# Optimization experiments

Hardware: AMD Instinct MI355X
Metric: run time of the kernel (lower is better)

## Reference

```python
import jax, jax.numpy as jnp
import numpy as np
import math

DIM = 768
HEADS = 12
HEAD_DIM = DIM // HEADS
SCALE_PARAM_INIT = 1.0 / math.sqrt(DIM)  # Scale(scale=1/sqrt(dim), init=1.0)


def cosine_norm(x, eps=1e-6):
    norm = jnp.maximum(jnp.linalg.norm(x, axis=-1, keepdims=True), eps)
    return x / norm


def setup_inputs() -> dict:
    key = jax.random.key(0)
    ks = jax.random.split(key, 6)
    B, N = 8, 1024
    x = jax.random.normal(ks[0], (B, N, DIM), dtype=jnp.float32)
    # torch nn.Linear weights are [out, in]; y = x @ W^T
    std = 1.0 / math.sqrt(DIM)
    Wq = jax.random.uniform(ks[1], (DIM, DIM), jnp.float32, -std, std)
    Wk = jax.random.uniform(ks[2], (DIM, DIM), jnp.float32, -std, std)
    Wv = jax.random.uniform(ks[3], (DIM, DIM), jnp.float32, -std, std)
    Wo = jax.random.uniform(ks[4], (DIM, DIM), jnp.float32, -std, std)
    # Scale param s: ones * scale, perturbed slightly for generality
    s_qk = SCALE_PARAM_INIT * (1.0 + 0.1 * jax.random.normal(ks[5], (HEADS, HEAD_DIM), jnp.float32))
    return {"x": x, "Wq": Wq, "Wk": Wk, "Wv": Wv, "Wo": Wo, "s_qk": s_qk}


def reference(x, Wq, Wk, Wv, Wo, s_qk):
    B, N, _ = x.shape
    # projections (torch Linear: x @ W^T)
    q = (x @ Wq.T).reshape(B, N, HEADS, HEAD_DIM)
    k = (x @ Wk.T).reshape(B, N, HEADS, HEAD_DIM)
    v = (x @ Wv.T).reshape(B, N, HEADS, HEAD_DIM)
    # effective scale = s * (init / scale)
    s_eff = s_qk * (1.0 / SCALE_PARAM_INIT)  # [H, D]
    q = cosine_norm(q) * s_eff  # broadcast over [B, N, H, D]
    k = cosine_norm(k) * s_eff
    scale = HEAD_DIM ** 0.5  # note: multiplies logits (nGPT-style)
    # [B, H, N, N]
    logits = jnp.einsum('bqhd,bkhd->bhqk', q, k) * scale
    attn = jax.nn.softmax(logits, axis=-1)
    out = jnp.einsum('bhqk,bkhd->bqhd', attn, v).reshape(B, N, HEADS * HEAD_DIM)
    return out @ Wo.T
```

## Files before the change

### kernel.cpp

```cpp
#include <hip/hip_runtime.h>
#include <hip/hip_bf16.h>
#include <math.h>

#define NDIM 768
#define NHEADS 12
#define HD 64
#define SEQ 1024
#define BATCH 8
#define MROWS (BATCH * SEQ)
#define SQRT_DIM 27.712812921102035f
#define LOG2E 1.4426950408889634f

typedef unsigned short u16;
typedef unsigned int u32;
typedef __attribute__((ext_vector_type(8))) short short8;
typedef __attribute__((ext_vector_type(4))) short bf16x4;
typedef __attribute__((ext_vector_type(4))) float f32x4;
typedef __attribute__((ext_vector_type(16))) float f32x16;

#define MFMA16(a, b, c) __builtin_amdgcn_mfma_f32_16x16x32_bf16(a, b, c, 0, 0, 0)
#define MFMA32(a, b, c) __builtin_amdgcn_mfma_f32_32x32x16_bf16(a, b, c, 0, 0, 0)

#if __has_builtin(__builtin_amdgcn_exp2f)
#define EXP2(x) __builtin_amdgcn_exp2f(x)
#else
#define EXP2(x) exp2f(x)
#endif

__device__ inline u16 f2bf(float f) {
    __hip_bfloat16 h = __float2bfloat16(f);
    return *reinterpret_cast<u16*>(&h);
}

__device__ inline u32 rne_pack(float a, float b) {
    u32 ua = __builtin_bit_cast(u32, a), ub = __builtin_bit_cast(u32, b);
    ua = (ua + 0x7fffu + ((ua >> 16) & 1u)) >> 16;
    ub = (ub + 0x7fffu + ((ub >> 16) & 1u)) >> 16;
    return (ub << 16) | ua;
}

__device__ inline void gl2lds16(const void* g, void* l) {
    __builtin_amdgcn_global_load_lds((const __attribute__((address_space(1))) void*)g,
                                     (__attribute__((address_space(3))) void*)l, 16, 0, 0);
}

__device__ inline void bar() {
    asm volatile("" ::: "memory");
    __builtin_amdgcn_s_barrier();
    asm volatile("" ::: "memory");
}
#define LGKM0 asm volatile("s_waitcnt lgkmcnt(0)" ::: "memory")
#define VM0   asm volatile("s_waitcnt vmcnt(0)" ::: "memory")

__global__ __launch_bounds__(256) void castall(const float* __restrict__ x,
                                               const float* __restrict__ Wq,
                                               const float* __restrict__ Wk,
                                               const float* __restrict__ Wv,
                                               const float* __restrict__ Wo,
                                               u16* __restrict__ xb,
                                               u16* __restrict__ Wqkv,
                                               u16* __restrict__ Wob) {
    const int WB = (NDIM * NDIM) / 1024;
    int blk = blockIdx.x;
    const float* s;
    u16* d;
    int base;
    if (blk < 6144) {
        s = x; d = xb; base = blk * 1024;
    } else {
        int wsel = (blk - 6144) / WB, r = (blk - 6144) % WB;
        base = r * 1024;
        if (wsel == 0)      { s = Wq; d = Wqkv; }
        else if (wsel == 1) { s = Wk; d = Wqkv + NDIM * NDIM; }
        else if (wsel == 2) { s = Wv; d = Wqkv + 2 * NDIM * NDIM; }
        else                { s = Wo; d = Wob; }
    }
    int i = base + threadIdx.x * 4;
    float4 v = *(const float4*)(s + i);
    uint2 o = make_uint2(rne_pack(v.x, v.y), rne_pack(v.z, v.w));
    *(uint2*)(d + i) = o;
}

__global__ __launch_bounds__(512, 2) void gemm256_qkv(const u16* __restrict__ A,
                                                      const u16* __restrict__ B,
                                                      u16* __restrict__ Vt,
                                                      const float* __restrict__ s_qk,
                                                      u16* __restrict__ Qdst,
                                                      u16* __restrict__ Kdst) {
    constexpr int K = NDIM;
    constexpr int NT = K / 64;
    __shared__ __align__(16) u16 As[2][2][128 * 64];
    __shared__ __align__(16) u16 Bs[2][2][128 * 64];

    const int t = threadIdx.x;
    const int wave = t >> 6, lane = t & 63;
    const int quad = lane >> 4, l16 = lane & 15;
    const int fx = l16 & 7;
    const int blk = blockIdx.x;

    const int srow = lane >> 3;
    const int schk = (lane & 7) ^ srow;
    auto stg = [&](const u16* src, u16* dst) {
#pragma unroll
        for (int it = 0; it < 2; ++it) {
            const int cb = it * 512 + wave * 64;
            const int r = (cb >> 3) + srow;
            gl2lds16(src + (size_t)r * K + schk * 8, (char*)dst + cb * 16);
        }
    };

    if (blk < 256) {
        const int wm = wave >> 2, wn = wave & 3;
        const int xcd = blk & 7, local = blk >> 3;
        const int bm = xcd * 1024 + (local >> 3) * 256;
        const int bn = (local & 7) * 256;

        f32x4 acc[8][4];
#pragma unroll
        for (int i = 0; i < 8; ++i)
#pragma unroll
            for (int j = 0; j < 4; ++j) acc[i][j] = (f32x4){0.f, 0.f, 0.f, 0.f};

        const u16* Ag = A + (size_t)bm * K;
        const u16* Bg = B + (size_t)bn * K;

        stg(Ag,                        As[0][0]);
        stg(Ag + (size_t)128 * K,      As[0][1]);
        stg(Bg,                        Bs[0][0]);
        stg(Bg + (size_t)128 * K,      Bs[0][1]);
        stg(Bg + 64,                   Bs[1][0]);
        stg(Bg + (size_t)128 * K + 64, Bs[1][1]);
        asm volatile("s_waitcnt vmcnt(4)" ::: "memory");
        bar();

        short8 a[4][2], b0[2][2], b1[2][2];
        const int rb0 = (wn & 1) * 64;

#pragma unroll 2
        for (int T = 0; T < NT; ++T) {
            const int db = T & 1;
            u16* Asl = As[db][wm];
            u16* Bsl = Bs[db][wn >> 1];
            const u16* An = Ag + (size_t)(T + 1) * 64;
            const u16* Bn = Bg + (size_t)(T + 2) * 64;

#pragma unroll
            for (int mi = 0; mi < 4; ++mi) {
                const int r = mi * 16 + l16;
#pragma unroll
                for (int kk = 0; kk < 2; ++kk)
                    a[mi][kk] = *(const short8*)&Asl[(r * 8 + ((kk * 4 + quad) ^ fx)) * 8];
            }
#pragma unroll
            for (int ni = 0; ni < 2; ++ni) {
                const int r = rb0 + ni * 16 + l16;
#pragma unroll
                for (int kk = 0; kk < 2; ++kk)
                    b0[ni][kk] = *(const short8*)&Bsl[(r * 8 + ((kk * 4 + quad) ^ fx)) * 8];
            }
            if (T + 1 < NT) stg(An, As[db ^ 1][0]);
            bar();
            LGKM0;
            __builtin_amdgcn_s_setprio(1);
#pragma unroll
            for (int kk = 0; kk < 2; ++kk)
#pragma unroll
                for (int mi = 0; mi < 4; ++mi)
#pragma unroll
                    for (int ni = 0; ni < 2; ++ni)
                        acc[mi][ni] = MFMA16(a[mi][kk], b0[ni][kk], acc[mi][ni]);
            __builtin_amdgcn_s_setprio(0);
            bar();

#pragma unroll
            for (int ni = 0; ni < 2; ++ni) {
                const int r = rb0 + (ni + 2) * 16 + l16;
#pragma unroll
                for (int kk = 0; kk < 2; ++kk)
                    b1[ni][kk] = *(const short8*)&Bsl[(r * 8 + ((kk * 4 + quad) ^ fx)) * 8];
            }
            if (T + 1 < NT) stg(An + (size_t)128 * K, As[db ^ 1][1]);
            bar();
            LGKM0;
            __builtin_amdgcn_s_setprio(1);
#pragma unroll
            for (int kk = 0; kk < 2; ++kk)
#pragma unroll
                for (int mi = 0; mi < 4; ++mi)
#pragma unroll
                    for (int ni = 0; ni < 2; ++ni)
                        acc[mi][ni + 2] = MFMA16(a[mi][kk], b1[ni][kk], acc[mi][ni + 2]);
            __builtin_amdgcn_s_setprio(0);
            bar();

#pragma unroll
            for (int mi = 0; mi < 4; ++mi) {
                const int r = (mi + 4) * 16 + l16;
#pragma unroll
                for (int kk = 0; kk < 2; ++kk)
                    a[mi][kk] = *(const short8*)&Asl[(r * 8 + ((kk * 4 + quad) ^ fx)) * 8];
            }
            if (T + 2 < NT) stg(Bn, Bs[db][0]);
            bar();
            LGKM0;
            __builtin_amdgcn_s_setprio(1);
#pragma unroll
            for (int kk = 0; kk < 2; ++kk)
#pragma unroll
                for (int mi = 0; mi < 4; ++mi)
#pragma unroll
                    for (int ni = 0; ni < 2; ++ni)
                        acc[mi + 4][ni + 2] = MFMA16(a[mi][kk], b1[ni][kk], acc[mi + 4][ni + 2]);
            __builtin_amdgcn_s_setprio(0);
            bar();

            if (T + 2 < NT) stg(Bn + (size_t)128 * K, Bs[db][1]);
            bar();
            __builtin_amdgcn_s_setprio(1);
#pragma unroll
            for (int kk = 0; kk < 2; ++kk)
#pragma unroll
                for (int mi = 0; mi < 4; ++mi)
#pragma unroll
                    for (int ni = 0; ni < 2; ++ni)
                        acc[mi + 4][ni] = MFMA16(a[mi][kk], b0[ni][kk], acc[mi + 4][ni]);
            __builtin_amdgcn_s_setprio(0);
            if (T + 2 < NT) {
                asm volatile("s_waitcnt vmcnt(4)" ::: "memory");
            } else {
                VM0;
            }
            bar();
        }

        const int cg = (bn + wn * 64) >> 6;
        if (cg >= 2 * NHEADS) {
            const int h = cg - 2 * NHEADS;
#pragma unroll
            for (int mi = 0; mi < 8; ++mi) {
                const int row = bm + wm * 128 + mi * 16 + quad * 4;
                const int bb = row >> 10, n0 = row & 1023;
#pragma unroll
                for (int ni = 0; ni < 4; ++ni) {
                    const int dd = ni * 16 + l16;
                    uint2 pk = make_uint2(rne_pack(acc[mi][ni][0], acc[mi][ni][1]),
                                          rne_pack(acc[mi][ni][2], acc[mi][ni][3]));
                    *(uint2*)(Vt + (((size_t)(bb * NHEADS + h) * HD + dd) << 10) + n0) = pk;
                }
            }
        } else {
            const bool isq = cg < NHEADS;
            const int h = isq ? cg : cg - NHEADS;
            u16* dst = isq ? Qdst : Kdst;
            const float ex = isq ? 8.f * LOG2E : 1.f;
            float sq[4];
#pragma unroll
            for (int ni = 0; ni < 4; ++ni)
                sq[ni] = s_qk[h * HD + ni * 16 + l16] * SQRT_DIM * ex;
#pragma unroll
            for (int mi = 0; mi < 8; ++mi)
#pragma unroll
                for (int r = 0; r < 4; ++r) {
                    float ss = 0.f;
#pragma unroll
                    for (int ni = 0; ni < 4; ++ni) ss += acc[mi][ni][r] * acc[mi][ni][r];
                    ss += __shfl_xor(ss, 1, 64);
                    ss += __shfl_xor(ss, 2, 64);
                    ss += __shfl_xor(ss, 4, 64);
                    ss += __shfl_xor(ss, 8, 64);
                    float inv = 1.f / fmaxf(sqrtf(ss), 1e-6f);
                    const int row = bm + wm * 128 + mi * 16 + quad * 4 + r;
                    const int bb = row >> 10, tok = row & 1023;
                    u16* o = dst + ((size_t)(bb * NHEADS + h) * SEQ + tok) * HD;
#pragma unroll
                    for (int ni = 0; ni < 4; ++ni)
                        o[ni * 16 + l16] = f2bf(acc[mi][ni][r] * sq[ni] * inv);
                }
        }
    } else {
        const int q = blk - 256;
        const int bm = (q >> 1) * 128;
        const int bn = 2048 + (q & 1) * 128;
        const int wm4 = wave >> 1, wn2 = wave & 1;
        const u16* Aq = A + (size_t)bm * K;
        const u16* Bq = B + (size_t)bn * K;

        f32x4 qa[2][4];
#pragma unroll
        for (int i = 0; i < 2; ++i)
#pragma unroll
            for (int j = 0; j < 4; ++j) qa[i][j] = (f32x4){0.f, 0.f, 0.f, 0.f};

        stg(Aq, As[0][0]);
        stg(Bq, Bs[0][0]);
        VM0;
        bar();
#pragma unroll 2
        for (int T = 0; T < NT; ++T) {
            const int db = T & 1;
            if (T + 1 < NT) {
                stg(Aq + (size_t)(T + 1) * 64, As[db ^ 1][0]);
                stg(Bq + (size_t)(T + 1) * 64, Bs[db ^ 1][0]);
            }
            const u16* Asl = As[db][0];
            const u16* Bsl = Bs[db][0];
            short8 af[2][2], bf[4][2];
#pragma unroll
            for (int mi = 0; mi < 2; ++mi) {
                const int r = wm4 * 32 + mi * 16 + l16;
#pragma unroll
                for (int kk = 0; kk < 2; ++kk)
                    af[mi][kk] = *(const short8*)&Asl[(r * 8 + ((kk * 4 + quad) ^ fx)) * 8];
            }
#pragma unroll
            for (int ni = 0; ni < 4; ++ni) {
                const int r = wn2 * 64 + ni * 16 + l16;
#pragma unroll
                for (int kk = 0; kk < 2; ++kk)
                    bf[ni][kk] = *(const short8*)&Bsl[(r * 8 + ((kk * 4 + quad) ^ fx)) * 8];
            }
            __builtin_amdgcn_s_setprio(1);
#pragma unroll
            for (int kk = 0; kk < 2; ++kk)
#pragma unroll
                for (int mi = 0; mi < 2; ++mi)
#pragma unroll
                    for (int ni = 0; ni < 4; ++ni)
                        qa[mi][ni] = MFMA16(af[mi][kk], bf[ni][kk], qa[mi][ni]);
            __builtin_amdgcn_s_setprio(0);
            VM0;
            bar();
        }
        const int h = 8 + (q & 1) * 2 + wn2;
#pragma unroll
        for (int mi = 0; mi < 2; ++mi) {
            const int row = bm + wm4 * 32 + mi * 16 + quad * 4;
            const int bb = row >> 10, n0 = row & 1023;
#pragma unroll
            for (int ni = 0; ni < 4; ++ni) {
                const int dd = ni * 16 + l16;
                uint2 pk = make_uint2(rne_pack(qa[mi][ni][0], qa[mi][ni][1]),
                                      rne_pack(qa[mi][ni][2], qa[mi][ni][3]));
                *(uint2*)(Vt + (((size_t)(bb * NHEADS + h) * HD + dd) << 10) + n0) = pk;
            }
        }
    }
}

template <int EPI>
__global__ __launch_bounds__(256) void gemm_bf16(const u16* __restrict__ A,
                                                 const u16* __restrict__ B,
                                                 void* __restrict__ C, int N,
                                                 const float* __restrict__ s_qk,
                                                 u16* __restrict__ Qdst,
                                                 u16* __restrict__ Kdst,
                                                 int NX) {
    constexpr int K = NDIM;
    constexpr int NKT = K / 32;
    __shared__ __align__(16) u16 As[2][4096];
    __shared__ __align__(16) u16 Bs[2][4096];
    const int t = threadIdx.x;
    const int wave = t >> 6, lane = t & 63;
    const int quad = lane >> 4, l16 = lane & 15;
    const int wx = (wave & 1) * 64, wy = (wave >> 1) * 64;
    const int blk = blockIdx.x;
    const int xcd = blk & 7, local = blk >> 3;
    const int bm = (xcd * 8 + local / NX) * 128;
    const int bn = (local % NX) * 128;

    f32x4 acc[4][4];
#pragma unroll
    for (int i = 0; i < 4; ++i)
#pragma unroll
        for (int j = 0; j < 4; ++j) acc[i][j] = (f32x4){0.f, 0.f, 0.f, 0.f};

    const int srl = lane >> 2;
    const int skc = (lane & 3) ^ ((lane >> 3) & 3);
    auto stage = [&](int k0, int bsel) {
#pragma unroll
        for (int it = 0; it < 2; ++it) {
            const int cb = it * 256 + wave * 64;
            const int row = (cb >> 6) * 16 + srl;
            gl2lds16(A + (size_t)(bm + row) * K + k0 + skc * 8,
                     (char*)As[bsel] + cb * 16);
            gl2lds16(B + (size_t)(bn + row) * K + k0 + skc * 8,
                     (char*)Bs[bsel] + cb * 16);
        }
    };
    const int fxor = (l16 >> 1) & 3;

    stage(0, 0);
#pragma unroll
    for (int kt = 0; kt < NKT; ++kt) {
        __syncthreads();
        if (kt + 1 < NKT) stage((kt + 1) * 32, (kt + 1) & 1);
        const int b = kt & 1;
        short8 af[4], bfr[4];
#pragma unroll
        for (int i = 0; i < 4; ++i)
            af[i] = *(const short8*)&As[b][
                ((((wy >> 4) + i) * 64 + l16 * 4 + (quad ^ fxor)) * 8)];
#pragma unroll
        for (int j = 0; j < 4; ++j)
            bfr[j] = *(const short8*)&Bs[b][
                ((((wx >> 4) + j) * 64 + l16 * 4 + (quad ^ fxor)) * 8)];
#pragma unroll
        for (int i = 0; i < 4; ++i)
#pragma unroll
            for (int j = 0; j < 4; ++j) acc[i][j] = MFMA16(af[i], bfr[j], acc[i][j]);
    }

    if constexpr (EPI == 0) {
#pragma unroll
        for (int i = 0; i < 4; ++i)
#pragma unroll
            for (int j = 0; j < 4; ++j)
#pragma unroll
                for (int r = 0; r < 4; ++r) {
                    const int row = bm + wy + i * 16 + quad * 4 + r;
                    const int col = bn + wx + j * 16 + l16;
                    ((float*)C)[(size_t)row * N + col] = acc[i][j][r];
                }
    }
}

__global__ __launch_bounds__(256) void attn_mfma(const u16* __restrict__ Qh,
                                                 const u16* __restrict__ Kh,
                                                 const u16* __restrict__ Vt,
                                                 u16* __restrict__ AO) {
    __shared__ __align__(16) u16 Ks[512 * 8];
    __shared__ __align__(16) u16 Vs[512 * 8];
    __shared__ __align__(16) u16 Ps[4 * 32 * 64];

    const int t = threadIdx.x;
    const int wave = t >> 6, lane = t & 63;
    const int l31 = lane & 31, half = lane >> 5;
    const int b = blockIdx.z, h = blockIdx.y, q0 = blockIdx.x * 128;
    const int bh = b * NHEADS + h;
    const u16* Kb = Kh + (size_t)bh * SEQ * HD;
    const u16* Vb = Vt + (size_t)bh * HD * SEQ;
    const int qb = q0 + wave * 32;
    const int pbase = wave * 2048 + l31 * 64;
    const int sw = (l31 & 15);

    short8 qf[4];
#pragma unroll
    for (int tt = 0; tt < 4; ++tt)
        qf[tt] = *(const short8*)(Qh + ((size_t)bh * SEQ + qb + l31) * HD +
                                  tt * 16 + half * 8);

    f32x16 o[2];
#pragma unroll
    for (int dt = 0; dt < 2; ++dt)
#pragma unroll
        for (int r = 0; r < 16; ++r) o[dt][r] = 0.f;
    float lp = 0.f;

    const int arl = lane >> 3;
    const int acc8 = (lane & 7) ^ arl;
    const int fx8 = l31 & 7;

    for (int j0 = 0; j0 < SEQ; j0 += 64) {
        __syncthreads();
#pragma unroll
        for (int it = 0; it < 2; ++it) {
            const int cb = it * 256 + wave * 64;
            const int r0 = (cb >> 6) * 8 + arl;
            gl2lds16(Kb + (size_t)(j0 + r0) * HD + acc8 * 8, (char*)Ks + cb * 16);
            gl2lds16(Vb + (size_t)r0 * SEQ + j0 + acc8 * 8, (char*)Vs + cb * 16);
        }
        asm volatile("s_waitcnt vmcnt(0)" ::: "memory");
        __syncthreads();

#pragma unroll
        for (int kt = 0; kt < 2; ++kt) {
            f32x16 sa;
#pragma unroll
            for (int r = 0; r < 16; ++r) sa[r] = 0.f;
#pragma unroll
            for (int tt = 0; tt < 4; ++tt) {
                short8 kf = *(const short8*)&Ks[
                    (((kt * 4 + (l31 >> 3)) * 64) + fx8 * 8 +
                     ((2 * tt + half) ^ fx8)) * 8];
                sa = MFMA32(kf, qf[tt], sa);
            }
#pragma unroll
            for (int rg = 0; rg < 4; ++rg) {
                float p0 = EXP2(sa[rg * 4 + 0]);
                float p1 = EXP2(sa[rg * 4 + 1]);
                float p2 = EXP2(sa[rg * 4 + 2]);
                float p3 = EXP2(sa[rg * 4 + 3]);
                lp += (p0 + p1) + (p2 + p3);
                uint2 pk = make_uint2(rne_pack(p0, p1), rne_pack(p2, p3));
                const int u = kt * 8 + rg * 2 + half;
                *(uint2*)&Ps[pbase + (u ^ sw) * 4] = pk;
            }
        }

#pragma unroll
        for (int k2 = 0; k2 < 4; ++k2) {
            const int u0 = k2 * 4 + half * 2;
            bf16x4 lo = *(const bf16x4*)&Ps[pbase + ((u0 + 0) ^ sw) * 4];
            bf16x4 hi = *(const bf16x4*)&Ps[pbase + ((u0 + 1) ^ sw) * 4];
            short8 pf = __builtin_shufflevector(lo, hi, 0, 1, 2, 3, 4, 5, 6, 7);
#pragma unroll
            for (int dt = 0; dt < 2; ++dt) {
                short8 vf = *(const short8*)&Vs[
                    (((dt * 4 + (l31 >> 3)) * 64) + fx8 * 8 +
                     ((2 * k2 + half) ^ fx8)) * 8];
                o[dt] = MFMA32(vf, pf, o[dt]);
            }
        }
    }

    const float invl = 1.f / (lp + __shfl_xor(lp, 32, 64));
    u16* ob = AO + (size_t)(b * SEQ + qb + l31) * NDIM + h * HD;
#pragma unroll
    for (int dt = 0; dt < 2; ++dt)
#pragma unroll
        for (int rg = 0; rg < 4; ++rg) {
            bf16x4 ok = {(short)f2bf(o[dt][rg * 4 + 0] * invl),
                         (short)f2bf(o[dt][rg * 4 + 1] * invl),
                         (short)f2bf(o[dt][rg * 4 + 2] * invl),
                         (short)f2bf(o[dt][rg * 4 + 3] * invl)};
            *(bf16x4*)(ob + dt * 32 + rg * 8 + half * 4) = ok;
        }
}

extern "C" void kernel_launch(void* const* d_in, const int* in_sizes, int n_in,
                              void* d_out, int out_size, void* d_ws, size_t ws_size,
                              hipStream_t stream) {
    const float* x    = (const float*)d_in[0];
    const float* Wq   = (const float*)d_in[1];
    const float* Wk   = (const float*)d_in[2];
    const float* Wv   = (const float*)d_in[3];
    const float* Wo   = (const float*)d_in[4];
    const float* s_qk = (const float*)d_in[5];
    float* out = (float*)d_out;

    char* w = (char*)d_ws;
    const size_t TE = (size_t)MROWS * NDIM;
    u16* xb   = (u16*)w;                    w += TE * 2;
    u16* Wqkv = (u16*)w;                    w += (size_t)3 * NDIM * NDIM * 2;
    u16* Wob  = (u16*)w;                    w += (size_t)NDIM * NDIM * 2;
    u16* Qh   = (u16*)w;                    w += TE * 2;
    u16* Kh   = (u16*)w;                    w += TE * 2;
    u16* Vt   = (u16*)w;                    w += TE * 2;
    u16* ao   = (u16*)w;

    castall<<<6144 + 4 * 576, 256, 0, stream>>>(x, Wq, Wk, Wv, Wo, xb, Wqkv, Wob);

    gemm256_qkv<<<384, 512, 0, stream>>>(xb, Wqkv, Vt, s_qk, Qh, Kh);

    attn_mfma<<<dim3(SEQ / 128, NHEADS, BATCH), 256, 0, stream>>>(Qh, Kh, Vt, ao);

    gemm_bf16<0><<<6 * 64, 256, 0, stream>>>(
        ao, Wob, out, NDIM, nullptr, nullptr, nullptr, 6);
}
```

Before: 192.4 us.

## Double-buffer K/V tiles, keep P in registers via permlane swap, remap blocks per XCD

The attention kernel now double-buffers the K and V LDS tiles, so the next tile's global-to-LDS load overlaps compute on the current one, and each iteration needs one barrier instead of two. The softmax probabilities are no longer written to and read back from LDS. They are packed to bf16 and rearranged between lane halves with permlane32_swap (shuffle fallback) to form the PV MFMA operand directly. The grid is flattened and remapped so that all query blocks of a given batch-head land on the same XCD, which should improve L2 reuse of K and V. These changes add LDS use for the second buffer and extra cross-lane operations.

```diff
diff --git a/kernel.cpp b/kernel.cpp
--- a/kernel.cpp
+++ b/kernel.cpp
@@ -17,6 +17,8 @@
 typedef __attribute__((ext_vector_type(4))) short bf16x4;
 typedef __attribute__((ext_vector_type(4))) float f32x4;
 typedef __attribute__((ext_vector_type(16))) float f32x16;
+typedef __attribute__((ext_vector_type(2))) u32 u32x2;
+typedef __attribute__((ext_vector_type(4))) u32 u32x4;
 
 #define MFMA16(a, b, c) __builtin_amdgcn_mfma_f32_16x16x32_bf16(a, b, c, 0, 0, 0)
 #define MFMA32(a, b, c) __builtin_amdgcn_mfma_f32_32x32x16_bf16(a, b, c, 0, 0, 0)
@@ -51,6 +53,17 @@
 }
 #define LGKM0 asm volatile("s_waitcnt lgkmcnt(0)" ::: "memory")
 #define VM0   asm volatile("s_waitcnt vmcnt(0)" ::: "memory")
+
+__device__ inline void plswap(u32 a, u32 b, int half, u32& x, u32& y) {
+#if __has_builtin(__builtin_amdgcn_permlane32_swap)
+    u32x2 r = __builtin_amdgcn_permlane32_swap(a, b, false, false);
+    x = r[0]; y = r[1];
+#else
+    u32 oa = __shfl_xor(a, 32, 64), ob = __shfl_xor(b, 32, 64);
+    x = half ? ob : a;
+    y = half ? b : oa;
+#endif
+}
 
 __global__ __launch_bounds__(256) void castall(const float* __restrict__ x,
                                                const float* __restrict__ Wq,
@@ -428,20 +441,22 @@
                                                  const u16* __restrict__ Kh,
                                                  const u16* __restrict__ Vt,
                                                  u16* __restrict__ AO) {
-    __shared__ __align__(16) u16 Ks[512 * 8];
-    __shared__ __align__(16) u16 Vs[512 * 8];
-    __shared__ __align__(16) u16 Ps[4 * 32 * 64];
+    __shared__ __align__(16) u16 Ks[2][512 * 8];
+    __shared__ __align__(16) u16 Vs[2][512 * 8];
 
     const int t = threadIdx.x;
     const int wave = t >> 6, lane = t & 63;
     const int l31 = lane & 31, half = lane >> 5;
-    const int b = blockIdx.z, h = blockIdx.y, q0 = blockIdx.x * 128;
-    const int bh = b * NHEADS + h;
+
+    const int bid = blockIdx.x;
+    const int xcd = bid & 7, idx = bid >> 3;
+    const int bh = xcd * 12 + (idx % 12);
+    const int q0 = (idx / 12) * 128;
+    const int b = bh / NHEADS, h = bh - b * NHEADS;
+
     const u16* Kb = Kh + (size_t)bh * SEQ * HD;
     const u16* Vb = Vt + (size_t)bh * HD * SEQ;
     const int qb = q0 + wave * 32;
-    const int pbase = wave * 2048 + l31 * 64;
-    const int sw = (l31 & 15);
 
     short8 qf[4];
 #pragma unroll
@@ -460,17 +475,26 @@
     const int acc8 = (lane & 7) ^ arl;
     const int fx8 = l31 & 7;
 
-    for (int j0 = 0; j0 < SEQ; j0 += 64) {
-        __syncthreads();
+    auto stage = [&](int j0, int db) {
 #pragma unroll
         for (int it = 0; it < 2; ++it) {
             const int cb = it * 256 + wave * 64;
             const int r0 = (cb >> 6) * 8 + arl;
-            gl2lds16(Kb + (size_t)(j0 + r0) * HD + acc8 * 8, (char*)Ks + cb * 16);
-            gl2lds16(Vb + (size_t)r0 * SEQ + j0 + acc8 * 8, (char*)Vs + cb * 16);
-        }
-        asm volatile("s_waitcnt vmcnt(0)" ::: "memory");
-        __syncthreads();
+            gl2lds16(Kb + (size_t)(j0 + r0) * HD + acc8 * 8,
+                     (char*)Ks[db] + cb * 16);
+            gl2lds16(Vb + (size_t)r0 * SEQ + j0 + acc8 * 8,
+                     (char*)Vs[db] + cb * 16);
+        }
+    };
+
+    stage(0, 0);
+    for (int jt = 0; jt < SEQ / 64; ++jt) {
+        const int db = jt & 1;
+        VM0;
+        bar();
+        if (jt + 1 < SEQ / 64) stage((jt + 1) * 64, db ^ 1);
+        const u16* Ksl = Ks[db];
+        const u16* Vsl = Vs[db];
 
 #pragma unroll
         for (int kt = 0; kt < 2; ++kt) {
@@ -479,36 +503,39 @@
             for (int r = 0; r < 16; ++r) sa[r] = 0.f;
 #pragma unroll
             for (int tt = 0; tt < 4; ++tt) {
-                short8 kf = *(const short8*)&Ks[
+                short8 kf = *(const short8*)&Ksl[
                     (((kt * 4 + (l31 >> 3)) * 64) + fx8 * 8 +
                      ((2 * tt + half) ^ fx8)) * 8];
                 sa = MFMA32(kf, qf[tt], sa);
             }
-#pragma unroll
-            for (int rg = 0; rg < 4; ++rg) {
-                float p0 = EXP2(sa[rg * 4 + 0]);
-                float p1 = EXP2(sa[rg * 4 + 1]);
-                float p2 = EXP2(sa[rg * 4 + 2]);
-                float p3 = EXP2(sa[rg * 4 + 3]);
-                lp += (p0 + p1) + (p2 + p3);
-                uint2 pk = make_uint2(rne_pack(p0, p1), rne_pack(p2, p3));
-                const int u = kt * 8 + rg * 2 + half;
-                *(uint2*)&Ps[pbase + (u ^ sw) * 4] = pk;
-            }
-        }
-
-#pragma unroll
-        for (int k2 = 0; k2 < 4; ++k2) {
-            const int u0 = k2 * 4 + half * 2;
-            bf16x4 lo = *(const bf16x4*)&Ps[pbase + ((u0 + 0) ^ sw) * 4];
-            bf16x4 hi = *(const bf16x4*)&Ps[pbase + ((u0 + 1) ^ sw) * 4];
-            short8 pf = __builtin_shufflevector(lo, hi, 0, 1, 2, 3, 4, 5, 6, 7);
-#pragma unroll
-            for (int dt = 0; dt < 2; ++dt) {
-                short8 vf = *(const short8*)&Vs[
-                    (((dt * 4 + (l31 >> 3)) * 64) + fx8 * 8 +
-                     ((2 * k2 + half) ^ fx8)) * 8];
-                o[dt] = MFMA32(vf, pf, o[dt]);
+            float p[16];
+#pragma unroll
+            for (int r = 0; r < 16; ++r) p[r] = EXP2(sa[r]);
+#pragma unroll
+            for (int rg = 0; rg < 4; ++rg)
+                lp += (p[rg * 4] + p[rg * 4 + 1]) + (p[rg * 4 + 2] + p[rg * 4 + 3]);
+            u32 q[8];
+#pragma unroll
+            for (int i = 0; i < 8; ++i) q[i] = rne_pack(p[2 * i], p[2 * i + 1]);
+            u32 d0, d1, d2, d3, e0, e1, e2, e3;
+            plswap(q[0], q[2], half, d0, d2);
+            plswap(q[1], q[3], half, d1, d3);
+            plswap(q[4], q[6], half, e0, e2);
+            plswap(q[5], q[7], half, e1, e3);
+            u32x4 f0v = {d0, d1, d2, d3};
+            u32x4 f1v = {e0, e1, e2, e3};
+            short8 pf0 = __builtin_bit_cast(short8, f0v);
+            short8 pf1 = __builtin_bit_cast(short8, f1v);
+#pragma unroll
+            for (int s = 0; s < 2; ++s) {
+                short8 pf = s ? pf1 : pf0;
+                const int c = kt * 4 + s * 2 + half;
+#pragma unroll
+                for (int dt = 0; dt < 2; ++dt) {
+                    short8 vf = *(const short8*)&Vsl[
+                        (((dt * 4 + (l31 >> 3)) * 64) + fx8 * 8 + (c ^ fx8)) * 8];
+                    o[dt] = MFMA32(vf, pf, o[dt]);
+                }
             }
         }
     }
@@ -552,7 +579,7 @@
 
     gemm256_qkv<<<384, 512, 0, stream>>>(xb, Wqkv, Vt, s_qk, Qh, Kh);
 
-    attn_mfma<<<dim3(SEQ / 128, NHEADS, BATCH), 256, 0, stream>>>(Qh, Kh, Vt, ao);
+    attn_mfma<<<768, 256, 0, stream>>>(Qh, Kh, Vt, ao);
 
     gemm_bf16<0><<<6 * 64, 256, 0, stream>>>(
         ao, Wob, out, NDIM, nullptr, nullptr, nullptr, 6);
```

After: 190.3 us. Within noise of the previous version (-1.1%).
